# Optimization experiments

Hardware: AMD Instinct MI355X
Metric: run time of the kernel (lower is better)

Reference implementation:

```python
import jax, jax.numpy as jnp
import numpy as np

# OpenCV GaussianBlur with ksize=3, sigma=0 uses the fixed small-kernel table
# [0.25, 0.5, 0.25] (separable), with border mode BORDER_REFLECT_101, which
# corresponds to jnp.pad(mode='reflect').
K0, K1 = 0.25, 0.5

def setup_inputs() -> dict:
    key = jax.random.key(0)
    x = jax.random.normal(key, (64, 3, 512, 512), dtype=jnp.float32)
    return {"x": x}

def _blur(x):
    # x: [B, C, H, W]; separable 1-2-1 / 4 filter along H then W.
    xp = jnp.pad(x, ((0, 0), (0, 0), (1, 1), (0, 0)), mode='reflect')
    x = K0 * xp[:, :, :-2, :] + K1 * xp[:, :, 1:-1, :] + K0 * xp[:, :, 2:, :]
    xp = jnp.pad(x, ((0, 0), (0, 0), (0, 0), (1, 1)), mode='reflect')
    x = K0 * xp[:, :, :, :-2] + K1 * xp[:, :, :, 1:-1] + K0 * xp[:, :, :, 2:]
    return x

def reference(x):
    return _blur(x)
```

## Files before the change

kernel.cpp:

```cpp
#include <hip/hip_runtime.h>


#define HH 512
#define WW 512

typedef float f4 __attribute__((ext_vector_type(4)));

#define VBLUR(d, m, c, pq)                         \
    d.x = 0.25f * (m.x + pq.x) + 0.5f * c.x;       \
    d.y = 0.25f * (m.y + pq.y) + 0.5f * c.y;       \
    d.z = 0.25f * (m.z + pq.z) + 0.5f * c.z;       \
    d.w = 0.25f * (m.w + pq.w) + 0.5f * c.w;

#define HBLUR(oa, ob, ua, ub, l, r)                \
    oa.x = 0.25f * (l    + ua.y) + 0.5f * ua.x;    \
    oa.y = 0.25f * (ua.x + ua.z) + 0.5f * ua.y;    \
    oa.z = 0.25f * (ua.y + ua.w) + 0.5f * ua.z;    \
    oa.w = 0.25f * (ua.z + ub.x) + 0.5f * ua.w;    \
    ob.x = 0.25f * (ua.w + ub.y) + 0.5f * ub.x;    \
    ob.y = 0.25f * (ub.x + ub.z) + 0.5f * ub.y;    \
    ob.z = 0.25f * (ub.y + ub.w) + 0.5f * ub.z;    \
    ob.w = 0.25f * (ub.z + r   ) + 0.5f * ub.w;

#define ROW_FINISH(ua, ub, h)                                        \
    {                                                                \
        float l = __shfl_up(ub.w, 1);                                \
        float r = __shfl_down(ua.x, 1);                              \
        if (lane == 0)  l = ua.y;                                    \
        if (lane == 63) r = ub.z;                                    \
        f4 oa, ob;                                                   \
        HBLUR(oa, ob, ua, ub, l, r)                                  \
        f4* S = (f4*)(q + (size_t)(h) * WW + w0);                    \
        __builtin_nontemporal_store(oa, S);                          \
        __builtin_nontemporal_store(ob, S + 1);                      \
    }

__global__ __launch_bounds__(256, 4) void gauss3_kernel(const float* __restrict__ in,
                                                        float* __restrict__ out) {
    int wid  = (blockIdx.x * 256 + threadIdx.x) >> 6;
    int lane = threadIdx.x & 63;

    int quad  = wid & 127;
    int plane = wid >> 7;

    int h0 = quad << 2;
    int hm = (h0 == 0)       ? 1      : h0 - 1;
    int hp = (h0 + 4 == HH)  ? HH - 2 : h0 + 4;

    const float* p = in  + (size_t)plane * (HH * WW);
    float*       q = out + (size_t)plane * (HH * WW);
    int w0 = lane << 3;

    const f4* Lm = (const f4*)(p + (size_t)hm       * WW + w0);
    const f4* L0 = (const f4*)(p + (size_t)h0       * WW + w0);
    const f4* L1 = (const f4*)(p + (size_t)(h0 + 1) * WW + w0);
    const f4* L2 = (const f4*)(p + (size_t)(h0 + 2) * WW + w0);
    const f4* L3 = (const f4*)(p + (size_t)(h0 + 3) * WW + w0);
    const f4* Lp = (const f4*)(p + (size_t)hp       * WW + w0);

    f4 ama = Lm[0], amb = Lm[1];
    f4 a0a = L0[0], a0b = L0[1];
    f4 a1a = L1[0], a1b = L1[1];
    f4 a2a = L2[0], a2b = L2[1];
    f4 a3a = L3[0], a3b = L3[1];
    f4 apa = Lp[0], apb = Lp[1];

    f4 ua, ub;
    VBLUR(ua, ama, a0a, a1a)  VBLUR(ub, amb, a0b, a1b)
    ROW_FINISH(ua, ub, h0)
    VBLUR(ua, a0a, a1a, a2a)  VBLUR(ub, a0b, a1b, a2b)
    ROW_FINISH(ua, ub, h0 + 1)
    VBLUR(ua, a1a, a2a, a3a)  VBLUR(ub, a1b, a2b, a3b)
    ROW_FINISH(ua, ub, h0 + 2)
    VBLUR(ua, a2a, a3a, apa)  VBLUR(ub, a2b, a3b, apb)
    ROW_FINISH(ua, ub, h0 + 3)
}

extern "C" void kernel_launch(void* const* d_in, const int* in_sizes, int n_in,
                              void* d_out, int out_size, void* d_ws, size_t ws_size,
                              hipStream_t stream) {
    const float* x   = (const float*)d_in[0];
    float*       out = (float*)d_out;

    int n      = in_sizes[0];
    int planes = n / (HH * WW);
    int waves  = planes * (HH / 4);
    int blocks = waves / 4;

    gauss3_kernel<<<blocks, 256, 0, stream>>>(x, out);
}
```

Measured before the change: 76.31 us.

## Process three row-quads per wave with software-pipelined loads across quads

Each wave now handles three 4-row quads instead of one, launching a fixed 2048 blocks. The loads for the next quad are issued before the current quad is computed and stored, with sched_barriers fencing the stages, so memory latency overlaps with compute. Launch bounds drop to 3 waves per SIMD to make room for the extra registers. The hardcoded grid assumes exactly 64x3 planes of 512x512 and no longer derives its size from the input.

```diff
diff --git a/kernel.cpp b/kernel.cpp
--- a/kernel.cpp
+++ b/kernel.cpp
@@ -5,6 +5,10 @@
 #define WW 512
 
 typedef float f4 __attribute__((ext_vector_type(4)));
+
+struct Quad {
+    f4 ma, mb, a0a, a0b, a1a, a1b, a2a, a2b, a3a, a3b, pa, pb;
+};
 
 #define VBLUR(d, m, c, pq)                         \
     d.x = 0.25f * (m.x + pq.x) + 0.5f * c.x;       \
@@ -22,58 +26,70 @@
     ob.z = 0.25f * (ub.y + ub.w) + 0.5f * ub.z;    \
     ob.w = 0.25f * (ub.z + r   ) + 0.5f * ub.w;
 
-#define ROW_FINISH(ua, ub, h)                                        \
+#define ROW(ma_, mb_, ca_, cb_, pa_, pb_, S)                         \
     {                                                                \
+        f4 ua, ub;                                                   \
+        VBLUR(ua, ma_, ca_, pa_)                                     \
+        VBLUR(ub, mb_, cb_, pb_)                                     \
         float l = __shfl_up(ub.w, 1);                                \
         float r = __shfl_down(ua.x, 1);                              \
         if (lane == 0)  l = ua.y;                                    \
         if (lane == 63) r = ub.z;                                    \
         f4 oa, ob;                                                   \
         HBLUR(oa, ob, ua, ub, l, r)                                  \
-        f4* S = (f4*)(q + (size_t)(h) * WW + w0);                    \
-        __builtin_nontemporal_store(oa, S);                          \
-        __builtin_nontemporal_store(ob, S + 1);                      \
+        __builtin_nontemporal_store(oa, (S));                        \
+        __builtin_nontemporal_store(ob, (S) + 1);                    \
     }
 
-__global__ __launch_bounds__(256, 4) void gauss3_kernel(const float* __restrict__ in,
+__device__ __forceinline__ void load_quad(const float* __restrict__ in, int q,
+                                          int w0, Quad& Q) {
+    int plane = q >> 7;
+    int h0    = (q & 127) << 2;
+    int hm = (h0 == 0)      ? 1       : h0 - 1;
+    int hp = (h0 + 4 == HH) ? HH - 2  : h0 + 4;
+    const float* base = in + (size_t)plane * (HH * WW) + w0;
+    const f4* Lm = (const f4*)(base + (size_t)hm       * WW);
+    const f4* L0 = (const f4*)(base + (size_t)h0       * WW);
+    const f4* L1 = (const f4*)(base + (size_t)(h0 + 1) * WW);
+    const f4* L2 = (const f4*)(base + (size_t)(h0 + 2) * WW);
+    const f4* L3 = (const f4*)(base + (size_t)(h0 + 3) * WW);
+    const f4* Lp = (const f4*)(base + (size_t)hp       * WW);
+    Q.ma  = Lm[0]; Q.mb  = Lm[1];
+    Q.a0a = L0[0]; Q.a0b = L0[1];
+    Q.a1a = L1[0]; Q.a1b = L1[1];
+    Q.a2a = L2[0]; Q.a2b = L2[1];
+    Q.a3a = L3[0]; Q.a3b = L3[1];
+    Q.pa  = Lp[0]; Q.pb  = Lp[1];
+}
+
+__device__ __forceinline__ void comp_quad(float* __restrict__ out, int q,
+                                          int lane, int w0, const Quad& Q) {
+    int plane = q >> 7;
+    int h0    = (q & 127) << 2;
+    float* base = out + (size_t)plane * (HH * WW) + w0;
+    ROW(Q.ma,  Q.mb,  Q.a0a, Q.a0b, Q.a1a, Q.a1b, (f4*)(base + (size_t)h0       * WW))
+    ROW(Q.a0a, Q.a0b, Q.a1a, Q.a1b, Q.a2a, Q.a2b, (f4*)(base + (size_t)(h0 + 1) * WW))
+    ROW(Q.a1a, Q.a1b, Q.a2a, Q.a2b, Q.a3a, Q.a3b, (f4*)(base + (size_t)(h0 + 2) * WW))
+    ROW(Q.a2a, Q.a2b, Q.a3a, Q.a3b, Q.pa,  Q.pb,  (f4*)(base + (size_t)(h0 + 3) * WW))
+}
+
+__global__ __launch_bounds__(256, 3) void gauss3_kernel(const float* __restrict__ in,
                                                         float* __restrict__ out) {
     int wid  = (blockIdx.x * 256 + threadIdx.x) >> 6;
     int lane = threadIdx.x & 63;
+    int w0   = lane << 3;
 
-    int quad  = wid & 127;
-    int plane = wid >> 7;
+    int q0 = wid, q1 = wid + 8192, q2 = wid + 16384;
 
-    int h0 = quad << 2;
-    int hm = (h0 == 0)       ? 1      : h0 - 1;
-    int hp = (h0 + 4 == HH)  ? HH - 2 : h0 + 4;
-
-    const float* p = in  + (size_t)plane * (HH * WW);
-    float*       q = out + (size_t)plane * (HH * WW);
-    int w0 = lane << 3;
-
-    const f4* Lm = (const f4*)(p + (size_t)hm       * WW + w0);
-    const f4* L0 = (const f4*)(p + (size_t)h0       * WW + w0);
-    const f4* L1 = (const f4*)(p + (size_t)(h0 + 1) * WW + w0);
-    const f4* L2 = (const f4*)(p + (size_t)(h0 + 2) * WW + w0);
-    const f4* L3 = (const f4*)(p + (size_t)(h0 + 3) * WW + w0);
-    const f4* Lp = (const f4*)(p + (size_t)hp       * WW + w0);
-
-    f4 ama = Lm[0], amb = Lm[1];
-    f4 a0a = L0[0], a0b = L0[1];
-    f4 a1a = L1[0], a1b = L1[1];
-    f4 a2a = L2[0], a2b = L2[1];
-    f4 a3a = L3[0], a3b = L3[1];
-    f4 apa = Lp[0], apb = Lp[1];
-
-    f4 ua, ub;
-    VBLUR(ua, ama, a0a, a1a)  VBLUR(ub, amb, a0b, a1b)
-    ROW_FINISH(ua, ub, h0)
-    VBLUR(ua, a0a, a1a, a2a)  VBLUR(ub, a0b, a1b, a2b)
-    ROW_FINISH(ua, ub, h0 + 1)
-    VBLUR(ua, a1a, a2a, a3a)  VBLUR(ub, a1b, a2b, a3b)
-    ROW_FINISH(ua, ub, h0 + 2)
-    VBLUR(ua, a2a, a3a, apa)  VBLUR(ub, a2b, a3b, apb)
-    ROW_FINISH(ua, ub, h0 + 3)
+    Quad A, B, C;
+    load_quad(in, q0, w0, A);
+    load_quad(in, q1, w0, B);
+    __builtin_amdgcn_sched_barrier(0);
+    comp_quad(out, q0, lane, w0, A);
+    load_quad(in, q2, w0, C);
+    __builtin_amdgcn_sched_barrier(0);
+    comp_quad(out, q1, lane, w0, B);
+    comp_quad(out, q2, lane, w0, C);
 }
 
 extern "C" void kernel_launch(void* const* d_in, const int* in_sizes, int n_in,
@@ -82,10 +98,6 @@
     const float* x   = (const float*)d_in[0];
     float*       out = (float*)d_out;
 
-    int n      = in_sizes[0];
-    int planes = n / (HH * WW);
-    int waves  = planes * (HH / 4);
-    int blocks = waves / 4;
-
+    int blocks = 2048;
     gauss3_kernel<<<blocks, 256, 0, stream>>>(x, out);
 }
```

New measurement: 77.97 us. 1.02x slower.
